# Performance work log

Hardware: AMD Instinct MI355X
Metric: run time of the kernel (lower is better)

Reference implementation:

```python
import jax, jax.numpy as jnp
import numpy as np

B, LQ, LK, D = 16, 2048, 2048, 64
TEMPERATURE = 8.0


def setup_inputs() -> dict:
    key = jax.random.key(0)
    kq, kk, kv, kt, km = jax.random.split(key, 5)
    q = jax.random.normal(kq, (B, LQ, D), dtype=jnp.float32)
    k = jax.random.normal(kk, (B, LK, D), dtype=jnp.float32)
    v = jax.random.normal(kv, (B, LK, D), dtype=jnp.float32)
    # time differences are positive
    time_diff = jax.random.uniform(kt, (B, LQ, LK), dtype=jnp.float32)
    mask = jax.random.randint(km, (B, LQ, LK), 0, 2).astype(bool)
    time_plus_weight = jnp.zeros((1,), dtype=jnp.float32)
    time_mul_weight = jnp.ones((1,), dtype=jnp.float32)
    return {"q": q, "k": k, "v": v, "time_diff": time_diff, "mask": mask,
            "time_plus_weight": time_plus_weight, "time_mul_weight": time_mul_weight}


def reference(q, k, v, time_diff, mask, time_plus_weight, time_mul_weight):
    # attn = QK^T / temperature  -> [B, LQ, LK]
    attn = jnp.einsum("bqd,bkd->bqk", q, k) / TEMPERATURE
    # time-decay bias (global mean/max over the whole time_diff tensor)
    td = time_diff / jnp.mean(time_diff)
    td = td + jax.nn.softplus(time_plus_weight) * jnp.max(td)
    time_diff_weight = 1.0 / jnp.log(jnp.exp(jnp.float32(1.0)) + td)
    attn = attn + time_mul_weight * time_diff_weight
    attn = jnp.where(mask, jnp.float32(-1e10), attn)
    attn = jax.nn.softmax(attn, axis=2)
    # dropout is identity in eval / p-effective-0 reference
    output = jnp.einsum("bqk,bkd->bqd", attn, v)
    return (output, attn)
```

## Files before the change

kernel.cpp:

```cpp
#include <hip/hip_runtime.h>
#include <hip/hip_bf16.h>

#define B_N 16
#define LQ_N 2048
#define LK_N 2048
#define D_N 64

typedef __attribute__((ext_vector_type(8))) __bf16 bf16x8;
typedef __attribute__((ext_vector_type(4))) float f32x4;
typedef __attribute__((ext_vector_type(2))) unsigned u32x2;
typedef __attribute__((ext_vector_type(4))) unsigned u32x4;

__device__ __forceinline__ unsigned cvt_pk_bf16(float lo, float hi) {
  unsigned r;
  asm("v_cvt_pk_bf16_f32 %0, %1, %2" : "=v"(r) : "v"(lo), "v"(hi));
  return r;
}

__device__ __forceinline__ void gl_lds16(const float* g, float* l) {
  __builtin_amdgcn_global_load_lds(
      (const __attribute__((address_space(1))) void*)g,
      (__attribute__((address_space(3))) void*)l, 16, 0, 0);
}

#define WAIT_VMC(N)  do { asm volatile("s_waitcnt vmcnt(" #N ")" ::: "memory"); __builtin_amdgcn_sched_barrier(0); } while (0)
#define WAIT_LGKM0() do { asm volatile("s_waitcnt lgkmcnt(0)" ::: "memory");    __builtin_amdgcn_sched_barrier(0); } while (0)
#define SBAR()       __builtin_amdgcn_sched_barrier(0)

__global__ __launch_bounds__(256) void red1_kernel(const float* __restrict__ td,
                                                   float* __restrict__ ws) {
  const int tid = threadIdx.x;
  const int gid = blockIdx.x * 256 + tid;
  float s = 0.f, mx = -1e30f;
  const float4* p = reinterpret_cast<const float4*>(td);
  for (int i = gid; i < 16777216; i += 524288) {
    float4 x = p[i];
    s += (x.x + x.y) + (x.z + x.w);
    mx = fmaxf(mx, fmaxf(fmaxf(x.x, x.y), fmaxf(x.z, x.w)));
  }
#pragma unroll
  for (int m = 1; m < 64; m <<= 1) {
    s += __shfl_xor(s, m, 64);
    mx = fmaxf(mx, __shfl_xor(mx, m, 64));
  }
  __shared__ float ss[4], sm[4];
  if ((tid & 63) == 0) { ss[tid >> 6] = s; sm[tid >> 6] = mx; }
  __syncthreads();
  if (tid == 0) {
    ws[blockIdx.x]        = (ss[0] + ss[1]) + (ss[2] + ss[3]);
    ws[2048 + blockIdx.x] = fmaxf(fmaxf(sm[0], sm[1]), fmaxf(sm[2], sm[3]));
  }
}

__global__ __launch_bounds__(256) void red2_kernel(const float* __restrict__ tpw,
                                                   const unsigned* __restrict__ mku,
                                                   float* __restrict__ ws) {
  const int tid = threadIdx.x;
  double s = 0.0; float mx = -1e30f;
  for (int i = tid; i < 2048; i += 256) { s += (double)ws[i]; mx = fmaxf(mx, ws[2048 + i]); }
#pragma unroll
  for (int m = 1; m < 64; m <<= 1) {
    s += __shfl_xor(s, m, 64);
    mx = fmaxf(mx, __shfl_xor(mx, m, 64));
  }
  unsigned big = 0;
  for (int i = tid; i < 1024; i += 256) big |= (mku[i] > 1u) ? 1u : 0u;
  const int anyw = __any(big != 0);
  __shared__ double sd[4]; __shared__ float sm[4]; __shared__ int sa[4];
  if ((tid & 63) == 0) { sd[tid >> 6] = s; sm[tid >> 6] = mx; sa[tid >> 6] = anyw; }
  __syncthreads();
  if (tid == 0) {
    double tot = (sd[0] + sd[1]) + (sd[2] + sd[3]);
    float m4 = fmaxf(fmaxf(sm[0], sm[1]), fmaxf(sm[2], sm[3]));
    double mean = tot / 67108864.0;
    float inv_mean = (float)(1.0 / mean);
    float sp = log1pf(__expf(tpw[0]));
    ws[4096] = inv_mean;
    ws[4097] = sp * m4 * inv_mean;
    ws[4098] = (sa[0] | sa[1] | sa[2] | sa[3]) ? 1.f : 0.f;
    ws[4099] = 2.718281828459045f + sp * m4 * inv_mean;
  }
}

__global__ __launch_bounds__(512)
void attn_kernel(
    const float* __restrict__ q, const float* __restrict__ kp, const float* __restrict__ vp,
    const float* __restrict__ td, const unsigned char* __restrict__ maskb,
    const float* __restrict__ tmwp, const float* __restrict__ ws,
    float* __restrict__ out, float* __restrict__ attn) {

  __shared__ float regA[8][2][1024];
  __shared__ float Qs[16 * 68];
  __shared__ unsigned short Ps[8][16 * 24];
  __shared__ float rsum[8][16];

  const int tid  = threadIdx.x;
  const int w    = tid >> 6;
  const int lane = tid & 63;
  const int lrow = lane & 15;
  const int lgrp = lane >> 4;

  const int b     = blockIdx.x >> 7;
  const int qbase = (blockIdx.x & 127) << 4;

  const float inv_mean = ws[4096];
  const float ec       = ws[4099];
  const float tmw      = tmwp[0];
  const float sc       = tmw * 2.0813689810056077f;
  const int   msh      = (ws[4098] != 0.f) ? 0 : 2;

  {
    const float qscale = 0.18033688011112042f;
    const int g = tid * 2, row = g >> 6, col = g & 63;
    const float* qp0 = q + ((size_t)(b * LQ_N + qbase + row) << 6) + col;
    Qs[row * 68 + col]     = qp0[0] * qscale;
    Qs[row * 68 + col + 1] = qp0[1] * qscale;
  }
  __syncthreads();

  bf16x8 qa[2];
#pragma unroll
  for (int h = 0; h < 2; ++h) {
    f32x4 a0 = *(const f32x4*)&Qs[lrow * 68 + h * 32 + lgrp * 8];
    f32x4 a1 = *(const f32x4*)&Qs[lrow * 68 + h * 32 + lgrp * 8 + 4];
    u32x4 kd = { cvt_pk_bf16(a0[0], a0[1]), cvt_pk_bf16(a0[2], a0[3]),
                 cvt_pk_bf16(a1[0], a1[1]), cvt_pk_bf16(a1[2], a1[3]) };
    qa[h] = __builtin_bit_cast(bf16x8, kd);
  }

  const unsigned qrow = (unsigned)(b * LQ_N + qbase + lrow);
  const unsigned tdo0 = (qrow << 11) + (unsigned)(w * 16 + lgrp * 4);
  const unsigned kvo0 = ((unsigned)b << 17) + ((unsigned)w << 10);
  const unsigned pA = (lgrp << 6) + ((lrow ^ lgrp)       << 2);
  const unsigned pB = (lgrp << 6) + ((lrow ^ (lgrp + 4)) << 2);

  auto dma16 = [&](const float* src_base, int c, int pb) {
    const unsigned base = kvo0 + (unsigned)c * 8192u;
    gl_lds16(src_base + (base         + pA), &regA[w][pb][0]);
    gl_lds16(src_base + (base +  256u + pB), &regA[w][pb][256]);
    gl_lds16(src_base + (base +  512u + pA), &regA[w][pb][512]);
    gl_lds16(src_base + (base +  768u + pB), &regA[w][pb][768]);
  };

  auto ldtd = [&](int c, f32x4* tdv, unsigned* mk4) {
    const unsigned to = tdo0 + (unsigned)c * 128u;
    *tdv = __builtin_nontemporal_load(reinterpret_cast<const f32x4*>(td + to));
    if (msh == 0) {
      *mk4 = *reinterpret_cast<const unsigned*>(maskb + to);
    } else {
      u32x4 m = __builtin_nontemporal_load(
          reinterpret_cast<const u32x4*>(maskb + ((size_t)to << 2)));
      *mk4 = (m[0] & 1u) | ((m[1] & 1u) << 8) | ((m[2] & 1u) << 16) | ((m[3] & 1u) << 24);
    }
  };

  dma16(kp, 0, 0); SBAR();
  dma16(kp, 1, 1); SBAR();
  f32x4    tdb[3];
  unsigned mkb[3];
  ldtd(0, &tdb[0], &mkb[0]); SBAR();
  ldtd(1, &tdb[1], &mkb[1]); SBAR();

  float rs = 0.f;
  u32x2 E[16];

#pragma unroll
  for (int c = 0; c < 16; ++c) {
    if (c == 0)       { WAIT_VMC(8);  }
    else if (c == 1)  { WAIT_VMC(10); }
    else if (c == 15) { WAIT_VMC(0);  }
    else              { WAIT_VMC(6);  }

    if (c < 14) { ldtd(c + 2, &tdb[(c + 2) % 3], &mkb[(c + 2) % 3]); SBAR(); }

    f32x4 acc = {0.f, 0.f, 0.f, 0.f};
#pragma unroll
    for (int h = 0; h < 2; ++h) {
      const int g0 = (h * 8 + lgrp * 2 + 0) ^ (lrow & 7);
      const int g1 = (h * 8 + lgrp * 2 + 1) ^ (lrow & 7);
      f32x4 ka = *(const f32x4*)&regA[w][c & 1][lrow * 64 + g0 * 4];
      f32x4 kc = *(const f32x4*)&regA[w][c & 1][lrow * 64 + g1 * 4];
      u32x4 kd = { cvt_pk_bf16(ka[0], ka[1]), cvt_pk_bf16(ka[2], ka[3]),
                   cvt_pk_bf16(kc[0], kc[1]), cvt_pk_bf16(kc[2], kc[3]) };
      acc = __builtin_amdgcn_mfma_f32_16x16x32_bf16(__builtin_bit_cast(bf16x8, kd), qa[h],
                                                    acc, 0, 0, 0);
    }
    WAIT_LGKM0();
    if (c < 14) { dma16(kp, c + 2, c & 1); SBAR(); }

    if (c == 0)       { WAIT_VMC(8);  }
    else if (c == 1)  { WAIT_VMC(12); }
    else if (c == 14) { WAIT_VMC(10); }
    else if (c == 15) { WAIT_VMC(0);  }
    else              { WAIT_VMC(16); }

    const f32x4    tv  = tdb[c % 3];
    const unsigned mk4 = mkb[c % 3];
    float e4[4];
#pragma unroll
    for (int i = 0; i < 4; ++i) {
      const float z  = __builtin_fmaf(tv[i], inv_mean, ec);
      const float l2 = __builtin_amdgcn_logf(z);
      const float r  = __builtin_amdgcn_rcpf(l2);
      const float sv = __builtin_fmaf(sc, r, acc[i]);
      const float e  = ((mk4 >> (8 * i)) & 0xffu) ? 0.f : __builtin_amdgcn_exp2f(sv);
      e4[i] = e;
      rs += e;
    }
    E[c] = u32x2{ cvt_pk_bf16(e4[0], e4[1]), cvt_pk_bf16(e4[2], e4[3]) };
  }

  dma16(vp, 0, 0); SBAR();
  dma16(vp, 1, 1); SBAR();

  rs += __shfl_xor(rs, 16, 64);
  rs += __shfl_xor(rs, 32, 64);
  if (lgrp == 0) rsum[w][lrow] = rs;
  __syncthreads();
  float invl;
  {
    float s = 0.f;
#pragma unroll
    for (int w2 = 0; w2 < 8; ++w2) s += rsum[w2][lrow];
    invl = __fdividef(1.f, s);
  }

  f32x4 oacc[4];
#pragma unroll
  for (int n = 0; n < 4; ++n) oacc[n] = {0.f, 0.f, 0.f, 0.f};

  const u32x4 zz = {0u, 0u, 0u, 0u};
#pragma unroll
  for (int c = 0; c < 16; ++c) {
    if (c == 0)       { WAIT_VMC(4); }
    else if (c == 1)  { WAIT_VMC(5); }
    else if (c == 15) { WAIT_VMC(2); }
    else              { WAIT_VMC(6); }

    const unsigned ex = E[c][0], ey = E[c][1];
    f32x4 pv;
    pv[0] = __uint_as_float(ex << 16)         * invl;
    pv[1] = __uint_as_float(ex & 0xffff0000u) * invl;
    pv[2] = __uint_as_float(ey << 16)         * invl;
    pv[3] = __uint_as_float(ey & 0xffff0000u) * invl;

    const unsigned d01 = cvt_pk_bf16(pv[0], pv[1]);
    const unsigned d23 = cvt_pk_bf16(pv[2], pv[3]);
    *reinterpret_cast<u32x2*>(&Ps[w][lrow * 24 + lgrp * 4]) = u32x2{ d01, d23 };

    bf16x8 pa;
    if (lgrp < 2) pa = *(const bf16x8*)&Ps[w][lrow * 24 + lgrp * 8];
    else          pa = __builtin_bit_cast(bf16x8, zz);

#pragma unroll
    for (int n = 0; n < 4; ++n) {
      u32x4 vd;
      if (lgrp < 2) {
        float vv[8];
#pragma unroll
        for (int e = 0; e < 8; ++e) {
          const int r    = lgrp * 8 + e;
          const int dcol = n * 16 + lrow;
          const int slot = (dcol >> 2) ^ (r & 7);
          vv[e] = regA[w][c & 1][r * 64 + slot * 4 + (dcol & 3)];
        }
        vd = u32x4{ cvt_pk_bf16(vv[0], vv[1]), cvt_pk_bf16(vv[2], vv[3]),
                    cvt_pk_bf16(vv[4], vv[5]), cvt_pk_bf16(vv[6], vv[7]) };
      } else {
        vd = zz;
      }
      oacc[n] = __builtin_amdgcn_mfma_f32_16x16x32_bf16(pa, __builtin_bit_cast(bf16x8, vd),
                                                        oacc[n], 0, 0, 0);
    }

    WAIT_LGKM0();
    if (c < 14) { dma16(vp, c + 2, c & 1); SBAR(); }

    __builtin_nontemporal_store(pv, reinterpret_cast<f32x4*>(attn + tdo0 + (unsigned)c * 128u));
  }

#pragma unroll
  for (int n = 0; n < 4; ++n)
#pragma unroll
    for (int i = 0; i < 4; ++i)
      regA[w][0][(lgrp * 4 + i) * 64 + n * 16 + lrow] = oacc[n][i];
  __syncthreads();
  for (int i2 = tid; i2 < 1024; i2 += 512) {
    float s = 0.f;
#pragma unroll
    for (int w2 = 0; w2 < 8; ++w2) s += regA[w2][0][i2];
    out[((size_t)(b * LQ_N + qbase) << 6) + i2] = s;
  }
}

extern "C" void kernel_launch(void* const* d_in, const int* in_sizes, int n_in,
                              void* d_out, int out_size, void* d_ws, size_t ws_size,
                              hipStream_t stream) {
  const float* q   = (const float*)d_in[0];
  const float* k   = (const float*)d_in[1];
  const float* v   = (const float*)d_in[2];
  const float* td  = (const float*)d_in[3];
  const unsigned char* mask = (const unsigned char*)d_in[4];
  const float* tpw = (const float*)d_in[5];
  const float* tmw = (const float*)d_in[6];
  float* out  = (float*)d_out;
  float* attn = out + (size_t)B_N * LQ_N * D_N;
  float* wsf  = (float*)d_ws;

  red1_kernel<<<2048, 256, 0, stream>>>(td, wsf);
  red2_kernel<<<1, 256, 0, stream>>>(tpw, (const unsigned*)mask, wsf);
  attn_kernel<<<2048, 512, 0, stream>>>(q, k, v, td, mask, tmw, wsf, out, attn);
}
```

Before: 313.3 us.

## Stage Q as bf16 in LDS and shorten time_diff prefetch depth

Q is now converted to bf16 once and kept in LDS, then reloaded per chunk instead of being held in registers as qa[2]. The time_diff/mask prefetch ring drops from 3 slots with a 2-ahead distance to 2 slots with a 1-ahead distance, and the vmcnt wait thresholds are rebalanced to match. The aim is to reduce register pressure so more waves fit or spills disappear. The cost is an extra LDS read per MFMA and less latency hiding for the streamed time_diff loads.

```diff
diff --git a/kernel.cpp b/kernel.cpp
--- a/kernel.cpp
+++ b/kernel.cpp
@@ -90,7 +90,7 @@
     float* __restrict__ out, float* __restrict__ attn) {
 
   __shared__ float regA[8][2][1024];
-  __shared__ float Qs[16 * 68];
+  __shared__ unsigned short Qsb[16 * 72];
   __shared__ unsigned short Ps[8][16 * 24];
   __shared__ float rsum[8][16];
 
@@ -109,24 +109,15 @@
   const float sc       = tmw * 2.0813689810056077f;
   const int   msh      = (ws[4098] != 0.f) ? 0 : 2;
 
-  {
+  if (tid < 256) {
     const float qscale = 0.18033688011112042f;
-    const int g = tid * 2, row = g >> 6, col = g & 63;
-    const float* qp0 = q + ((size_t)(b * LQ_N + qbase + row) << 6) + col;
-    Qs[row * 68 + col]     = qp0[0] * qscale;
-    Qs[row * 68 + col + 1] = qp0[1] * qscale;
-  }
-  __syncthreads();
-
-  bf16x8 qa[2];
-#pragma unroll
-  for (int h = 0; h < 2; ++h) {
-    f32x4 a0 = *(const f32x4*)&Qs[lrow * 68 + h * 32 + lgrp * 8];
-    f32x4 a1 = *(const f32x4*)&Qs[lrow * 68 + h * 32 + lgrp * 8 + 4];
-    u32x4 kd = { cvt_pk_bf16(a0[0], a0[1]), cvt_pk_bf16(a0[2], a0[3]),
-                 cvt_pk_bf16(a1[0], a1[1]), cvt_pk_bf16(a1[2], a1[3]) };
-    qa[h] = __builtin_bit_cast(bf16x8, kd);
-  }
+    const int row = tid >> 4, c4 = (tid & 15) << 2;
+    f32x4 x = *reinterpret_cast<const f32x4*>(q + ((size_t)(b * LQ_N + qbase + row) << 6) + c4);
+    *reinterpret_cast<u32x2*>(&Qsb[row * 72 + c4]) =
+        u32x2{ cvt_pk_bf16(x[0] * qscale, x[1] * qscale),
+               cvt_pk_bf16(x[2] * qscale, x[3] * qscale) };
+  }
+  __syncthreads();
 
   const unsigned qrow = (unsigned)(b * LQ_N + qbase + lrow);
   const unsigned tdo0 = (qrow << 11) + (unsigned)(w * 16 + lgrp * 4);
@@ -156,22 +147,18 @@
 
   dma16(kp, 0, 0); SBAR();
   dma16(kp, 1, 1); SBAR();
-  f32x4    tdb[3];
-  unsigned mkb[3];
+  f32x4    tdb[2];
+  unsigned mkb[2];
   ldtd(0, &tdb[0], &mkb[0]); SBAR();
-  ldtd(1, &tdb[1], &mkb[1]); SBAR();
 
   float rs = 0.f;
   u32x2 E[16];
 
 #pragma unroll
   for (int c = 0; c < 16; ++c) {
-    if (c == 0)       { WAIT_VMC(8);  }
-    else if (c == 1)  { WAIT_VMC(10); }
-    else if (c == 15) { WAIT_VMC(0);  }
-    else              { WAIT_VMC(6);  }
-
-    if (c < 14) { ldtd(c + 2, &tdb[(c + 2) % 3], &mkb[(c + 2) % 3]); SBAR(); }
+    if (c == 0)       { WAIT_VMC(6); }
+    else if (c == 15) { WAIT_VMC(4); }
+    else              { WAIT_VMC(8); }
 
     f32x4 acc = {0.f, 0.f, 0.f, 0.f};
 #pragma unroll
@@ -180,22 +167,22 @@
       const int g1 = (h * 8 + lgrp * 2 + 1) ^ (lrow & 7);
       f32x4 ka = *(const f32x4*)&regA[w][c & 1][lrow * 64 + g0 * 4];
       f32x4 kc = *(const f32x4*)&regA[w][c & 1][lrow * 64 + g1 * 4];
+      bf16x8 qv = *(const bf16x8*)&Qsb[lrow * 72 + h * 32 + lgrp * 8];
       u32x4 kd = { cvt_pk_bf16(ka[0], ka[1]), cvt_pk_bf16(ka[2], ka[3]),
                    cvt_pk_bf16(kc[0], kc[1]), cvt_pk_bf16(kc[2], kc[3]) };
-      acc = __builtin_amdgcn_mfma_f32_16x16x32_bf16(__builtin_bit_cast(bf16x8, kd), qa[h],
+      acc = __builtin_amdgcn_mfma_f32_16x16x32_bf16(__builtin_bit_cast(bf16x8, kd), qv,
                                                     acc, 0, 0, 0);
     }
     WAIT_LGKM0();
     if (c < 14) { dma16(kp, c + 2, c & 1); SBAR(); }
-
-    if (c == 0)       { WAIT_VMC(8);  }
-    else if (c == 1)  { WAIT_VMC(12); }
-    else if (c == 14) { WAIT_VMC(10); }
-    else if (c == 15) { WAIT_VMC(0);  }
-    else              { WAIT_VMC(16); }
-
-    const f32x4    tv  = tdb[c % 3];
-    const unsigned mk4 = mkb[c % 3];
+    if (c < 15) { ldtd(c + 1, &tdb[(c + 1) & 1], &mkb[(c + 1) & 1]); SBAR(); }
+
+    if (c <= 13)      { WAIT_VMC(6); }
+    else if (c == 14) { WAIT_VMC(2); }
+    else              { WAIT_VMC(0); }
+
+    const f32x4    tv  = tdb[c & 1];
+    const unsigned mk4 = mkb[c & 1];
     float e4[4];
 #pragma unroll
     for (int i = 0; i < 4; ++i) {
```

Result: slower. 322.2 us (+2.9%).
